# Kernel optimization log

Hardware: AMD Instinct MI355X
Metric: run time of the kernel (lower is better)

## Reference

```python
import jax, jax.numpy as jnp
import numpy as np
from jax import lax

L, C, H, W = 3, 64, 32, 32   # layer_num, new_size channels/spatial
N = H * W                    # 1024 attention positions
B = 8


def _conv(x, w, b, stride, pad):
    out = lax.conv_general_dilated(
        x, w, (stride, stride), [(pad, pad), (pad, pad)],
        dimension_numbers=('NCHW', 'OIHW', 'NCHW'))
    return out + b[None, :, None, None]


def setup_inputs() -> dict:
    key = jax.random.key(0)
    ks = iter(jax.random.split(key, 40))
    def rn(shape, scale=1.0):
        return (jax.random.normal(next(ks), shape) * scale).astype(jnp.float32)
    inp = {
        'src0': rn((B, 128, 64, 64)), 'src1': rn((B, 256, 32, 32)), 'src2': rn((B, 512, 32, 32)),
        'tgt0': rn((B, 128, 64, 64)), 'tgt1': rn((B, 256, 32, 32)), 'tgt2': rn((B, 512, 32, 32)),
    }
    # Project/Fit convs: layer0 is stride-2 3x3 (64->32), layers 1,2 are 1x1
    for pre, ic, k in [('fs0', 128, 3), ('fs1', 256, 1), ('fs2', 512, 1),
                       ('ft0', 128, 3), ('ft1', 256, 1), ('ft2', 512, 1)]:
        inp[pre + '_w'] = rn((C, ic, k, k), (ic * k * k) ** -0.5)
        inp[pre + '_b'] = rn((C,), 0.01)
    # PAM query/key/value and CAM value 1x1 convs, stacked over layers
    for pre in ['pq', 'pk', 'pv', 'cv']:
        inp[pre + '_w'] = rn((L, C, C), C ** -0.5)
        inp[pre + '_b'] = rn((L, C), 0.01)
    return inp


def reference(src0, src1, src2, tgt0, tgt1, tgt2,
              fs0_w, fs0_b, fs1_w, fs1_b, fs2_w, fs2_b,
              ft0_w, ft0_b, ft1_w, ft1_b, ft2_w, ft2_b,
              pq_w, pq_b, pk_w, pk_b, pv_w, pv_b, cv_w, cv_b):
    # Project: Fit each source/target to [B,C,H,W]
    S = jnp.stack([_conv(src0, fs0_w, fs0_b, 2, 1),
                   _conv(src1, fs1_w, fs1_b, 1, 0),
                   _conv(src2, fs2_w, fs2_b, 1, 0)])   # [L,B,C,H,W]
    T = jnp.stack([_conv(tgt0, ft0_w, ft0_b, 2, 1),
                   _conv(tgt1, ft1_w, ft1_b, 1, 0),
                   _conv(tgt2, ft2_w, ft2_b, 1, 0)])
    S = S.reshape(L, B, C, N)
    T = T.reshape(L, B, C, N)

    # ---- PAM: position attention over all (target i, source j) pairs ----
    q = jnp.einsum('ioc,ibcn->ibon', pq_w, T) + pq_b[:, None, :, None]
    k = jnp.einsum('joc,jbcn->jbon', pk_w, S) + pk_b[:, None, :, None]
    v = jnp.einsum('ioc,ibcn->ibon', pv_w, T) + pv_b[:, None, :, None]
    e_pam = jnp.einsum('ibcn,jbcm->ijbnm', q, k)          # [L,L,B,N,N]
    alpha_pam = jax.nn.softmax(lax.stop_gradient(e_pam.mean(axis=(2, 3, 4))), axis=-1)
    attn_pam = jax.nn.softmax(e_pam, axis=-1).sum(axis=1)  # sum over sources j -> [L,B,N,N]
    # out[b,c,n] = sum_m v[b,c,m] * attn[b,n,m]  (value @ attention^T)
    out_pam = jnp.einsum('ibcm,ibnm->ibcn', v, attn_pam)

    # ---- CAM: channel attention over all pairs ----
    e_cam = jnp.einsum('ibcn,jbdn->ijbcd', T, S)           # [L,L,B,C,C]
    alpha_cam = jax.nn.softmax(lax.stop_gradient(e_cam.mean(axis=(2, 3, 4))), axis=-1)
    attn_cam = jax.nn.softmax(e_cam, axis=-1).sum(axis=1)  # [L,B,C,C]
    vc = jnp.einsum('ioc,ibcn->ibon', cv_w, T) + cv_b[:, None, :, None]
    out_cam = jnp.einsum('ibcd,ibdn->ibcn', attn_cam, vc)

    fused = ((out_pam + out_cam) * 0.5).reshape(L, B, C * N)
    alpha = (alpha_cam + alpha_pam) * 0.5                  # [L,L]
    srcs = S.reshape(L, B, C * N)
    # DAAttention appends fused_i then projected target_i per layer (order preserved)
    tgts = jnp.stack([fused, T.reshape(L, B, C * N)], axis=1).reshape(2 * L, B, C * N)
    return (srcs, alpha, tgts)
```

## Files before the change

kernel.cpp:

```cpp
#include <hip/hip_runtime.h>

static constexpr int L_ = 3, B_ = 8, C_ = 64, N_ = 1024;
static constexpr int PLANE = C_ * N_;
static constexpr int SZ    = L_ * B_ * PLANE;
static constexpr int BPL   = B_ * PLANE;

#define DI __device__ __forceinline__

typedef _Float16 h8 __attribute__((ext_vector_type(8)));
typedef __attribute__((ext_vector_type(4))) float f32x4;
typedef unsigned int uint32;

DI float wred_sum(float v) {
#pragma unroll
  for (int m = 1; m < 64; m <<= 1) v += __shfl_xor(v, m, 64);
  return v;
}

DI unsigned short f2h(float f) {
  return __builtin_bit_cast(unsigned short, (_Float16)f);
}
DI float h2f(unsigned short h) {
  return (float)__builtin_bit_cast(_Float16, h);
}
DI uint32 pkh(float a, float b) {
  return (uint32)f2h(a) | ((uint32)f2h(b) << 16);
}
DI h8 bch8(uint4 v) { return __builtin_bit_cast(h8, v); }

DI f32x4 mfmah(h8 a, h8 b, f32x4 c) {
  return __builtin_amdgcn_mfma_f32_16x16x32_f16(a, b, c, 0, 0, 0);
}

__global__ __launch_bounds__(256) void xprep_kernel(
    const float* __restrict__ in, unsigned short* __restrict__ out, int K, int N)
{
  const int g = blockIdx.x, kc = blockIdx.y, nc = blockIdx.z;
  const int t = threadIdx.x;
  __shared__ float tl[64][65];
  const float* ing = in + (size_t)g * K * N + (size_t)(kc * 64) * N + nc * 64;
#pragma unroll 4
  for (int r = 0; r < 16; ++r) {
    const int kk = r * 4 + (t >> 6);
    tl[kk][t & 63] = ing[(size_t)kk * N + (t & 63)];
  }
  __syncthreads();
  const int mm = t >> 2, kseg = (t & 3) * 16;
  uint32 hw[8];
#pragma unroll
  for (int ii = 0; ii < 8; ++ii)
    hw[ii] = pkh(tl[kseg + 2 * ii][mm], tl[kseg + 2 * ii + 1][mm]);
  unsigned short* o = out + ((size_t)g * N + nc * 64 + mm) * K + kc * 64 + kseg;
  uint4 h0; h0.x = hw[0]; h0.y = hw[1]; h0.z = hw[2]; h0.w = hw[3];
  uint4 h1; h1.x = hw[4]; h1.y = hw[5]; h1.z = hw[6]; h1.w = hw[7];
  *reinterpret_cast<uint4*>(o)     = h0;
  *reinterpret_cast<uint4*>(o + 8) = h1;
}

__global__ __launch_bounds__(256) void w9conv_kernel(
    const float* __restrict__ w_s, const float* __restrict__ w_t,
    unsigned short* __restrict__ w9_s, unsigned short* __restrict__ w9_t)
{
  const int e = blockIdx.x * 256 + threadIdx.x;
  const float* w = (e < 73728) ? w_s : w_t;
  unsigned short* o = (e < 73728) ? w9_s : w9_t;
  const int le = (e < 73728) ? e : e - 73728;
  const int ci = le & 127;
  const int q = le >> 7;
  const int co = q & 63;
  const int k9 = q >> 6;
  o[le] = f2h(w[(co * 128 + ci) * 9 + k9]);
}

__global__ __launch_bounds__(256) void conv0_mfma_kernel(
    const unsigned short* __restrict__ inT_s, const unsigned short* __restrict__ inT_t,
    const unsigned short* __restrict__ w9_s, const unsigned short* __restrict__ w9_t,
    const float* __restrict__ b_s, const float* __restrict__ b_t,
    float* __restrict__ Sout, float* __restrict__ Tout, float* __restrict__ tdup)
{
  const int yr = blockIdx.x;
  const int b  = blockIdx.y;
  const int st = blockIdx.z;
  const unsigned short* inT = st ? inT_t : inT_s;
  const unsigned short* w9  = st ? w9_t  : w9_s;
  const float* bias = st ? b_t : b_s;
  float* outA = st ? Tout : Sout;

  const int t = threadIdx.x, lane = t & 63;
  const int ct = t >> 6;
  const int nl = lane & 15, g16 = lane >> 4;
  const unsigned short* inb = inT + (size_t)b * (4096 * 128);
  const unsigned short* wbase = w9 + (size_t)(ct * 16 + nl) * 128;

  f32x4 acc0 = f32x4{0.f, 0.f, 0.f, 0.f};
  f32x4 acc1 = f32x4{0.f, 0.f, 0.f, 0.f};
  const uint4 zz = uint4{0u, 0u, 0u, 0u};

#pragma unroll 1
  for (int tap = 0; tap < 9; ++tap) {
    const int ky = tap / 3, kx = tap - 3 * (tap / 3);
    const int py = 2 * yr - 1 + ky;
    const int px0 = 2 * nl - 1 + kx;
    const int px1 = px0 + 32;
    const bool v0 = (py >= 0) && (px0 >= 0);
    const bool v1 = (py >= 0);
    const unsigned short* prow = inb + (ptrdiff_t)py * (64 * 128);
#pragma unroll
    for (int ks = 0; ks < 4; ++ks) {
      const h8 a = bch8(*reinterpret_cast<const uint4*>(
          wbase + tap * 8192 + ks * 32 + g16 * 8));
      const uint4 bv0 = v0 ? *reinterpret_cast<const uint4*>(
                                 prow + px0 * 128 + ks * 32 + g16 * 8) : zz;
      const uint4 bv1 = v1 ? *reinterpret_cast<const uint4*>(
                                 prow + px1 * 128 + ks * 32 + g16 * 8) : zz;
      acc0 = mfmah(a, bch8(bv0), acc0);
      acc1 = mfmah(a, bch8(bv1), acc1);
    }
  }

  const int yb = yr * 32;
#pragma unroll
  for (int r = 0; r < 4; ++r) {
    const int co = ct * 16 + g16 * 4 + r;
    const float bv = bias[co];
    const int idx = (b * 64 + co) * 1024 + yb + nl;
    const float o0 = acc0[r] + bv;
    const float o1 = acc1[r] + bv;
    outA[idx] = o0; outA[idx + 16] = o1;
    if (st) { tdup[idx] = o0; tdup[idx + 16] = o1; }
  }
}

__global__ __launch_bounds__(256) void gemm64_kernel(
    const float* __restrict__ W, int wstride, int wdiv,
    const float* __restrict__ X, int xstride,
    float* __restrict__ out, int ostride,
    const float* __restrict__ bias, int bstride,
    int K)
{
  const int g  = blockIdx.x;
  const int n0 = blockIdx.y * 64;
  const float* Wg = W + (size_t)(g / wdiv) * wstride;
  const float* Xg = X + (size_t)g * xstride;
  const int t = threadIdx.x;
  __shared__ float Xs[32][64];
  __shared__ float Ws[32][64];
  const int tn = t & 15, cgp = t >> 4;
  const int n4 = tn * 4, co4 = cgp * 4;
  float acc[4][4] = {};

  for (int k0 = 0; k0 < K; k0 += 32) {
    {
      const int kk = t >> 4;
      const int nn = (t & 15) * 4;
      *reinterpret_cast<float4*>(&Xs[kk][nn]) =
          *reinterpret_cast<const float4*>(Xg + (size_t)(k0 + kk) * N_ + n0 + nn);
      *reinterpret_cast<float4*>(&Xs[kk + 16][nn]) =
          *reinterpret_cast<const float4*>(Xg + (size_t)(k0 + kk + 16) * N_ + n0 + nn);
    }
    {
      const int co = t & 63, q4 = t >> 6;
      const float* wp = Wg + (size_t)co * K + k0 + q4 * 8;
      const float4 a = *reinterpret_cast<const float4*>(wp);
      const float4 c = *reinterpret_cast<const float4*>(wp + 4);
      const int kb = q4 * 8;
      Ws[kb + 0][co] = a.x; Ws[kb + 1][co] = a.y; Ws[kb + 2][co] = a.z; Ws[kb + 3][co] = a.w;
      Ws[kb + 4][co] = c.x; Ws[kb + 5][co] = c.y; Ws[kb + 6][co] = c.z; Ws[kb + 7][co] = c.w;
    }
    __syncthreads();
#pragma unroll
    for (int kk = 0; kk < 32; ++kk) {
      const float4 xv = *reinterpret_cast<const float4*>(&Xs[kk][n4]);
      const float4 wv = *reinterpret_cast<const float4*>(&Ws[kk][co4]);
      const float xa[4] = {xv.x, xv.y, xv.z, xv.w};
      const float wa[4] = {wv.x, wv.y, wv.z, wv.w};
#pragma unroll
      for (int a = 0; a < 4; ++a)
#pragma unroll
        for (int b2 = 0; b2 < 4; ++b2)
          acc[a][b2] = fmaf(wa[a], xa[b2], acc[a][b2]);
    }
    __syncthreads();
  }

  float bv[4] = {0.f, 0.f, 0.f, 0.f};
  if (bias) {
    const float* bg = bias + (size_t)(g / wdiv) * bstride;
    bv[0] = bg[co4]; bv[1] = bg[co4 + 1]; bv[2] = bg[co4 + 2]; bv[3] = bg[co4 + 3];
  }
#pragma unroll
  for (int ii = 0; ii < 4; ++ii) {
    float4 o4;
    o4.x = acc[ii][0] + bv[ii]; o4.y = acc[ii][1] + bv[ii];
    o4.z = acc[ii][2] + bv[ii]; o4.w = acc[ii][3] + bv[ii];
    *reinterpret_cast<float4*>(out + (size_t)g * ostride + (co4 + ii) * N_ + n0 + n4) = o4;
  }
}

__global__ __launch_bounds__(256) void proj_kernel(
    const float* __restrict__ Tm, const float* __restrict__ Sm,
    const float* __restrict__ wq, const float* __restrict__ wk,
    const float* __restrict__ wv2, const float* __restrict__ wc,
    const float* __restrict__ bq, const float* __restrict__ bk,
    const float* __restrict__ bv2, const float* __restrict__ bc,
    float* __restrict__ outbase)
{
  const int g  = blockIdx.x;
  const int n0 = blockIdx.y * 64;
  const int z  = blockIdx.z;
  const float* W  = (z == 0) ? wq : (z == 1) ? wk : (z == 2) ? wv2 : wc;
  const float* bi = (z == 0) ? bq : (z == 1) ? bk : (z == 2) ? bv2 : bc;
  const float* Xg = ((z == 1) ? Sm : Tm) + (size_t)g * PLANE;
  float* out = outbase + (size_t)z * SZ + (size_t)g * PLANE;
  const float* Wg = W + (g >> 3) * 4096;
  const float* bg = bi + (g >> 3) * 64;

  const int t = threadIdx.x;
  __shared__ float Xs[32][64];
  __shared__ float Ws[32][64];
  const int tn = t & 15, cgp = t >> 4;
  const int n4 = tn * 4, co4 = cgp * 4;
  float acc[4][4] = {};

#pragma unroll 1
  for (int k0 = 0; k0 < 64; k0 += 32) {
    {
      const int kk = t >> 4;
      const int nn = (t & 15) * 4;
      *reinterpret_cast<float4*>(&Xs[kk][nn]) =
          *reinterpret_cast<const float4*>(Xg + (size_t)(k0 + kk) * N_ + n0 + nn);
      *reinterpret_cast<float4*>(&Xs[kk + 16][nn]) =
          *reinterpret_cast<const float4*>(Xg + (size_t)(k0 + kk + 16) * N_ + n0 + nn);
    }
    {
      const int co = t & 63, q4 = t >> 6;
      const float* wp = Wg + (size_t)co * 64 + k0 + q4 * 8;
      const float4 a = *reinterpret_cast<const float4*>(wp);
      const float4 c = *reinterpret_cast<const float4*>(wp + 4);
      const int kb = q4 * 8;
      Ws[kb + 0][co] = a.x; Ws[kb + 1][co] = a.y; Ws[kb + 2][co] = a.z; Ws[kb + 3][co] = a.w;
      Ws[kb + 4][co] = c.x; Ws[kb + 5][co] = c.y; Ws[kb + 6][co] = c.z; Ws[kb + 7][co] = c.w;
    }
    __syncthreads();
#pragma unroll
    for (int kk = 0; kk < 32; ++kk) {
      const float4 xv = *reinterpret_cast<const float4*>(&Xs[kk][n4]);
      const float4 wv = *reinterpret_cast<const float4*>(&Ws[kk][co4]);
      const float xa[4] = {xv.x, xv.y, xv.z, xv.w};
      const float wa[4] = {wv.x, wv.y, wv.z, wv.w};
#pragma unroll
      for (int a = 0; a < 4; ++a)
#pragma unroll
        for (int b2 = 0; b2 < 4; ++b2)
          acc[a][b2] = fmaf(wa[a], xa[b2], acc[a][b2]);
    }
    __syncthreads();
  }

#pragma unroll
  for (int ii = 0; ii < 4; ++ii) {
    const float bv = bg[co4 + ii];
    float4 o4;
    o4.x = acc[ii][0] + bv; o4.y = acc[ii][1] + bv;
    o4.z = acc[ii][2] + bv; o4.w = acc[ii][3] + bv;
    *reinterpret_cast<float4*>(out + (co4 + ii) * N_ + n0 + n4) = o4;
  }
}

__global__ __launch_bounds__(256) void whconv_kernel(
    const float* __restrict__ w1s, const float* __restrict__ w2s,
    const float* __restrict__ w1t, const float* __restrict__ w2t,
    unsigned short* __restrict__ wh)
{
  const int p = blockIdx.x * 256 + threadIdx.x;
  const float* in; int local; unsigned short* out;
  if (p < 8192)       { in = w1s; local = p;         out = wh; }
  else if (p < 24576) { in = w2s; local = p - 8192;  out = wh + 16384; }
  else if (p < 32768) { in = w1t; local = p - 24576; out = wh + 49152; }
  else                { in = w2t; local = p - 32768; out = wh + 65536; }
  const float2 v = *reinterpret_cast<const float2*>(in + 2 * local);
  *reinterpret_cast<uint32*>(out + 2 * local) = pkh(v.x, v.y);
}

__global__ __launch_bounds__(256) void gemmh_kernel(
    const unsigned short* __restrict__ Xa, const unsigned short* __restrict__ Xb,
    const unsigned short* __restrict__ Wa, const unsigned short* __restrict__ Wb,
    const float* __restrict__ ba, const float* __restrict__ bb,
    float* __restrict__ oa, float* __restrict__ ob, float* __restrict__ o2b,
    int K)
{
  const int g = blockIdx.x;
  const bool isb = g >= 8;
  const int gl = g & 7;
  const unsigned short* X = (isb ? Xb : Xa) + (size_t)gl * 1024 * K;
  const unsigned short* W = isb ? Wb : Wa;
  const float* bias = isb ? bb : ba;
  float* out = (isb ? ob : oa) + (size_t)gl * PLANE;
  float* out2 = isb ? o2b + (size_t)gl * PLANE : nullptr;

  const int t = threadIdx.x, lane = t & 63, wv = t >> 6;
  const int nl = lane & 15, g16 = lane >> 4;
  const int n0w = blockIdx.y * 64 + wv * 16;

  const unsigned short* xp = X + (size_t)(n0w + nl) * K + g16 * 8;
  const unsigned short* wp = W + (size_t)nl * K + g16 * 8;

  f32x4 acc[4];
#pragma unroll
  for (int ct = 0; ct < 4; ++ct) acc[ct] = f32x4{0.f, 0.f, 0.f, 0.f};

#pragma unroll 4
  for (int kk = 0; kk < K; kk += 32) {
    const h8 a = bch8(*reinterpret_cast<const uint4*>(xp + kk));
#pragma unroll
    for (int ct = 0; ct < 4; ++ct) {
      const h8 bfr = bch8(*reinterpret_cast<const uint4*>(wp + (size_t)ct * 16 * K + kk));
      acc[ct] = mfmah(a, bfr, acc[ct]);
    }
  }

#pragma unroll
  for (int ct = 0; ct < 4; ++ct) {
    const int co = ct * 16 + nl;
    const float bv = bias[co];
    float4 o4;
    o4.x = acc[ct][0] + bv; o4.y = acc[ct][1] + bv;
    o4.z = acc[ct][2] + bv; o4.w = acc[ct][3] + bv;
    const int idx = co * N_ + n0w + g16 * 4;
    *reinterpret_cast<float4*>(out + idx) = o4;
    if (out2) {
      out2[idx] = o4.x; out2[idx + 1] = o4.y;
      out2[idx + 2] = o4.z; out2[idx + 3] = o4.w;
    }
  }
}

__global__ __launch_bounds__(256) void kprep_kernel(
    const float* __restrict__ kb, const float* __restrict__ vb,
    unsigned short* __restrict__ kT, unsigned short* __restrict__ vh)
{
  const int g = blockIdx.x;
  const int ch = blockIdx.y;
  const int t = threadIdx.x;
  const float* kg = kb + (size_t)g * PLANE;
  __shared__ float tl[64][65];

#pragma unroll 1
  for (int tile = 0; tile < 4; ++tile) {
    const int m0 = ch * 256 + tile * 64;
    __syncthreads();
#pragma unroll 4
    for (int r = 0; r < 16; ++r) {
      const int c = r * 4 + (t >> 6);
      tl[c][t & 63] = kg[c * N_ + m0 + (t & 63)];
    }
    __syncthreads();
    const int mm = t >> 2, cseg = (t & 3) * 16;
    uint32 hw[8];
#pragma unroll
    for (int ii = 0; ii < 8; ++ii)
      hw[ii] = pkh(tl[cseg + 2 * ii][mm], tl[cseg + 2 * ii + 1][mm]);
    const size_t o = ((size_t)g * 1024 + m0 + mm) * 64 + cseg;
    uint4 h0; h0.x = hw[0]; h0.y = hw[1]; h0.z = hw[2]; h0.w = hw[3];
    uint4 h1; h1.x = hw[4]; h1.y = hw[5]; h1.z = hw[6]; h1.w = hw[7];
    *reinterpret_cast<uint4*>(kT + o)     = h0;
    *reinterpret_cast<uint4*>(kT + o + 8) = h1;
  }

  const float* vg = vb + (size_t)g * PLANE;
  unsigned short* vo = vh + (size_t)g * PLANE;
  for (int e8 = ch * 2048 + t; e8 < (ch + 1) * 2048; e8 += 256) {
    const float4 a = *reinterpret_cast<const float4*>(vg + (size_t)e8 * 8);
    const float4 b = *reinterpret_cast<const float4*>(vg + (size_t)e8 * 8 + 4);
    uint4 u;
    u.x = pkh(a.x, a.y); u.y = pkh(a.z, a.w);
    u.z = pkh(b.x, b.y); u.w = pkh(b.z, b.w);
    *reinterpret_cast<uint4*>(vo + (size_t)e8 * 8) = u;
  }
}

__global__ __launch_bounds__(256) void ecam_kernel(
    const float* __restrict__ T, const float* __restrict__ S,
    float* __restrict__ ecam, float* __restrict__ esum_cam)
{
  const int bx = blockIdx.x;
  const int b = bx & 7;
  const int j = (bx >> 3) % 3;
  const int i = bx / 24;
  const float* Tg = T + (size_t)(i * 8 + b) * PLANE;
  const float* Sg = S + (size_t)(j * 8 + b) * PLANE;
  const int t = threadIdx.x;
  __shared__ float Ts[64 * 68];
  __shared__ float Ss[64 * 68];
  __shared__ float rs[4];
  float acc[4][4] = {};
  const int c0 = (t & 15) * 4, d0 = (t >> 4) * 4;

  for (int nb = 0; nb < 1024; nb += 64) {
    __syncthreads();
    {
      const int nn = t & 63, rb = t >> 6;
#pragma unroll
      for (int r = 0; r < 16; ++r) {
        const int row = rb * 16 + r;
        Ts[nn * 68 + row] = Tg[row * N_ + nb + nn];
        Ss[nn * 68 + row] = Sg[row * N_ + nb + nn];
      }
    }
    __syncthreads();
#pragma unroll 8
    for (int nn = 0; nn < 64; ++nn) {
      const float4 tv = *reinterpret_cast<const float4*>(&Ts[nn * 68 + c0]);
      const float4 sv = *reinterpret_cast<const float4*>(&Ss[nn * 68 + d0]);
      const float ta[4] = {tv.x, tv.y, tv.z, tv.w};
      const float sa[4] = {sv.x, sv.y, sv.z, sv.w};
#pragma unroll
      for (int ci = 0; ci < 4; ++ci)
#pragma unroll
        for (int di = 0; di < 4; ++di)
          acc[ci][di] = fmaf(ta[ci], sa[di], acc[ci][di]);
    }
  }
  float s = 0.f;
#pragma unroll
  for (int ci = 0; ci < 4; ++ci)
#pragma unroll
    for (int di = 0; di < 4; ++di) s += acc[ci][di];
  s = wred_sum(s);
  if ((t & 63) == 0) rs[t >> 6] = s;
  __syncthreads();
  if (t == 0) atomicAdd(esum_cam + i * 3 + j, rs[0] + rs[1] + rs[2] + rs[3]);

  float* eo = ecam + (size_t)((i * 3 + j) * 8 + b) * 4096;
#pragma unroll
  for (int ci = 0; ci < 4; ++ci) {
    float4 o4; o4.x = acc[ci][0]; o4.y = acc[ci][1]; o4.z = acc[ci][2]; o4.w = acc[ci][3];
    *reinterpret_cast<float4*>(eo + (c0 + ci) * 64 + d0) = o4;
  }
}

__global__ __launch_bounds__(256) void acam_kernel(
    const float* __restrict__ ecam, float* __restrict__ acam)
{
  const int bx = blockIdx.x;
  const int b = bx & 7, i = bx >> 3;
  const int t = threadIdx.x;
  const int c = t >> 2, seg = t & 3;
  float acc[16] = {};
#pragma unroll
  for (int j = 0; j < 3; ++j) {
    const float* e = ecam + (size_t)((i * 3 + j) * 8 + b) * 4096 + c * 64 + seg * 16;
    float ev[16];
#pragma unroll
    for (int r = 0; r < 4; ++r) {
      const float4 v4 = *reinterpret_cast<const float4*>(e + r * 4);
      ev[4 * r] = v4.x; ev[4 * r + 1] = v4.y; ev[4 * r + 2] = v4.z; ev[4 * r + 3] = v4.w;
    }
    float mx = ev[0];
#pragma unroll
    for (int r = 1; r < 16; ++r) mx = fmaxf(mx, ev[r]);
    mx = fmaxf(mx, __shfl_xor(mx, 1, 4));
    mx = fmaxf(mx, __shfl_xor(mx, 2, 4));
    float pv[16], ss = 0.f;
#pragma unroll
    for (int r = 0; r < 16; ++r) { pv[r] = __expf(ev[r] - mx); ss += pv[r]; }
    ss += __shfl_xor(ss, 1, 4);
    ss += __shfl_xor(ss, 2, 4);
    const float rc = 1.f / ss;
#pragma unroll
    for (int r = 0; r < 16; ++r) acc[r] += pv[r] * rc;
  }
  float* ao = acam + (size_t)(i * 8 + b) * 4096 + c * 64 + seg * 16;
#pragma unroll
  for (int r = 0; r < 4; ++r) {
    float4 o4; o4.x = acc[4 * r]; o4.y = acc[4 * r + 1]; o4.z = acc[4 * r + 2]; o4.w = acc[4 * r + 3];
    *reinterpret_cast<float4*>(ao + r * 4) = o4;
  }
}

__global__ __launch_bounds__(512, 4) void pam_mfma_kernel(
    const float* __restrict__ q, const unsigned short* __restrict__ kT,
    const unsigned short* __restrict__ vh,
    const float* __restrict__ ocam, float* __restrict__ tgts, float* __restrict__ esum_pam)
{
  const int bx = blockIdx.x;
  const int qt = bx & 63;
  const int b  = (bx >> 6) & 7;
  const int i  = bx >> 9;
  const int n0 = qt * 16;
  const int t = threadIdx.x;
  const int lane = t & 63;
  const int wv = t >> 6;
  const int nl = lane & 15;
  const int g16 = lane >> 4;

  __shared__ unsigned short Plds[16 * 1024];
  __shared__ float qlds[64 * 17];
  __shared__ float redmx[128];
  __shared__ float redse[128];
  __shared__ float redes[8];
  float* osum = qlds;

  const size_t ibo = (size_t)(i * 8 + b) * PLANE;

  const float* qg = q + ibo;
  for (int e = t; e < 1024; e += 512)
    qlds[(e >> 4) * 17 + (e & 15)] = qg[(e >> 4) * N_ + n0 + (e & 15)];
  __syncthreads();

  h8 qh[2];
#pragma unroll
  for (int ks = 0; ks < 2; ++ks) {
#pragma unroll
    for (int idx = 0; idx < 8; ++idx)
      qh[ks][idx] = (_Float16)qlds[(ks * 32 + g16 * 8 + idx) * 17 + nl];
  }

  const int wm0 = wv * 128;
  const int ct = wv & 3;
  const int mh = wv >> 2;

#pragma unroll 1
  for (int j = 0; j < 3; ++j) {
    const unsigned short* kp =
        kT + ((size_t)(j * 8 + b) * 1024 + wm0 + nl) * 64 + g16 * 8;

    f32x4 l4[8];
#pragma unroll
    for (int hh = 0; hh < 2; ++hh) {
      uint4 kf[8];
#pragma unroll
      for (int tt = 0; tt < 4; ++tt) {
        const int off = (hh * 4 + tt) * 1024;
        kf[2 * tt]     = *reinterpret_cast<const uint4*>(kp + off);
        kf[2 * tt + 1] = *reinterpret_cast<const uint4*>(kp + off + 32);
      }
#pragma unroll
      for (int tt = 0; tt < 4; ++tt) {
        f32x4 a = f32x4{0.f, 0.f, 0.f, 0.f};
        a = mfmah(bch8(kf[2 * tt]), qh[0], a);
        a = mfmah(bch8(kf[2 * tt + 1]), qh[1], a);
        l4[hh * 4 + tt] = a;
      }
    }

    float pm = -3.4e38f, es = 0.f;
#pragma unroll
    for (int tt = 0; tt < 8; ++tt) {
#pragma unroll
      for (int r = 0; r < 4; ++r) { pm = fmaxf(pm, l4[tt][r]); es += l4[tt][r]; }
    }
    pm = fmaxf(pm, __shfl_xor(pm, 16, 64));
    pm = fmaxf(pm, __shfl_xor(pm, 32, 64));
    es = wred_sum(es);
    if (lane < 16) redmx[wv * 16 + lane] = pm;
    if (lane == 0) redes[wv] = es;
    __syncthreads();
    float mx = redmx[nl];
#pragma unroll
    for (int w = 1; w < 8; ++w) mx = fmaxf(mx, redmx[w * 16 + nl]);
    if (t == 0) {
      float s = 0.f;
#pragma unroll
      for (int w = 0; w < 8; ++w) s += redes[w];
      atomicAdd(esum_pam + i * 3 + j, s);
    }

    float ps = 0.f;
#pragma unroll
    for (int tt = 0; tt < 8; ++tt) {
#pragma unroll
      for (int r = 0; r < 4; ++r) {
        l4[tt][r] = __expf(l4[tt][r] - mx);
        ps += l4[tt][r];
      }
    }
    ps += __shfl_xor(ps, 16, 64);
    ps += __shfl_xor(ps, 32, 64);
    if (lane < 16) redse[wv * 16 + lane] = ps;
    __syncthreads();
    float den = redse[nl];
#pragma unroll
    for (int w = 1; w < 8; ++w) den += redse[w * 16 + nl];
    const float rs = 1.f / den;

#pragma unroll
    for (int tt = 0; tt < 8; ++tt) {
      const int m = wm0 + tt * 16 + g16 * 4;
      unsigned short* pp = &Plds[nl * 1024 + (m ^ (nl * 8))];
      float p0 = l4[tt][0] * rs, p1 = l4[tt][1] * rs;
      float p2 = l4[tt][2] * rs, p3 = l4[tt][3] * rs;
      if (j > 0) {
        const uint2 old = *reinterpret_cast<const uint2*>(pp);
        p0 += h2f((unsigned short)(old.x & 0xffffu));
        p1 += h2f((unsigned short)(old.x >> 16));
        p2 += h2f((unsigned short)(old.y & 0xffffu));
        p3 += h2f((unsigned short)(old.y >> 16));
      }
      uint2 w2; w2.x = pkh(p0, p1); w2.y = pkh(p2, p3);
      *reinterpret_cast<uint2*>(pp) = w2;
    }
  }

  __syncthreads();

  const unsigned short* vg = vh + ibo + (size_t)(ct * 16 + nl) * 1024 + mh * 512 + g16 * 8;
  f32x4 oa = f32x4{0.f, 0.f, 0.f, 0.f};
#pragma unroll
  for (int hh = 0; hh < 2; ++hh) {
    uint4 vf[8];
#pragma unroll
    for (int u = 0; u < 8; ++u)
      vf[u] = *reinterpret_cast<const uint4*>(vg + (hh * 8 + u) * 32);
#pragma unroll
    for (int u = 0; u < 8; ++u) {
      const int ml = mh * 512 + (hh * 8 + u) * 32 + g16 * 8;
      const uint4 pf = *reinterpret_cast<const uint4*>(&Plds[nl * 1024 + (ml ^ (nl * 8))]);
      oa = mfmah(bch8(vf[u]), bch8(pf), oa);
    }
  }

  if (mh == 0) {
#pragma unroll
    for (int r = 0; r < 4; ++r)
      osum[(ct * 16 + g16 * 4 + r) * 16 + nl] = oa[r];
  }
  __syncthreads();
  if (mh == 1) {
    const float* og = ocam + ibo;
    float* outg = tgts + (size_t)(2 * i * 8 + b) * PLANE;
#pragma unroll
    for (int r = 0; r < 4; ++r) {
      const int c = ct * 16 + g16 * 4 + r;
      const int idx = c * N_ + n0 + nl;
      outg[idx] = 0.5f * (oa[r] + osum[c * 16 + nl] + og[idx]);
    }
  }
}

__global__ void alpha_kernel(const float* __restrict__ esum, float* __restrict__ alpha)
{
  const int t = threadIdx.x;
  if (t >= 9) return;
  const int i = t / 3, j = t % 3;
  float p[3], c[3];
#pragma unroll
  for (int jj = 0; jj < 3; ++jj) {
    p[jj] = esum[i * 3 + jj] * (1.0f / 8388608.0f);
    c[jj] = esum[9 + i * 3 + jj] * (1.0f / 32768.0f);
  }
  const float mp = fmaxf(p[0], fmaxf(p[1], p[2]));
  const float mc = fmaxf(c[0], fmaxf(c[1], c[2]));
  float sp = 0.f, sc = 0.f;
#pragma unroll
  for (int jj = 0; jj < 3; ++jj) { sp += __expf(p[jj] - mp); sc += __expf(c[jj] - mc); }
  alpha[t] = 0.5f * (__expf(p[j] - mp) / sp + __expf(c[j] - mc) / sc);
}

extern "C" void kernel_launch(void* const* d_in, const int* in_sizes, int n_in,
                              void* d_out, int out_size, void* d_ws, size_t ws_size,
                              hipStream_t stream)
{
  const float* src0 = (const float*)d_in[0];
  const float* src1 = (const float*)d_in[1];
  const float* src2 = (const float*)d_in[2];
  const float* tgt0 = (const float*)d_in[3];
  const float* tgt1 = (const float*)d_in[4];
  const float* tgt2 = (const float*)d_in[5];
  const float* fs0_w = (const float*)d_in[6];  const float* fs0_b = (const float*)d_in[7];
  const float* fs1_w = (const float*)d_in[8];  const float* fs1_b = (const float*)d_in[9];
  const float* fs2_w = (const float*)d_in[10]; const float* fs2_b = (const float*)d_in[11];
  const float* ft0_w = (const float*)d_in[12]; const float* ft0_b = (const float*)d_in[13];
  const float* ft1_w = (const float*)d_in[14]; const float* ft1_b = (const float*)d_in[15];
  const float* ft2_w = (const float*)d_in[16]; const float* ft2_b = (const float*)d_in[17];
  const float* pq_w = (const float*)d_in[18];  const float* pq_b = (const float*)d_in[19];
  const float* pk_w = (const float*)d_in[20];  const float* pk_b = (const float*)d_in[21];
  const float* pv_w = (const float*)d_in[22];  const float* pv_b = (const float*)d_in[23];
  const float* cv_w = (const float*)d_in[24];  const float* cv_b = (const float*)d_in[25];

  float* out = (float*)d_out;
  float* S     = out;
  float* alpha = out + SZ;
  float* tgts  = out + SZ + 9;

  float* ws   = (float*)d_ws;
  float* T    = ws;
  float* qb   = ws + (size_t)SZ;
  float* kb   = ws + (size_t)2 * SZ;
  float* vb   = ws + (size_t)3 * SZ;
  float* vcb  = ws + (size_t)4 * SZ;
  float* ocam = ws + (size_t)5 * SZ;
  float* ecam = ws + (size_t)6 * SZ;
  float* acam = ws + (size_t)6 * SZ + 294912;
  float* esum = ws + (size_t)6 * SZ + 393216;

  unsigned short* kT = (unsigned short*)(ws + (size_t)6 * SZ + 393216 + 256);
  unsigned short* vh = kT + (size_t)24 * PLANE;
  unsigned short* wh = vh + (size_t)24 * PLANE;
  unsigned short* w9s = wh + 98304;
  unsigned short* w9t = w9s + 73728;

  unsigned short* inTs = (unsigned short*)qb;
  unsigned short* inTt = inTs + 4194304;
  unsigned short* Xs1 = (unsigned short*)qb;
  unsigned short* Xs2 = Xs1 + 2097152;
  unsigned short* Xt1 = Xs1 + 6291456;
  unsigned short* Xt2 = Xs1 + 8388608;

  hipMemsetAsync(esum, 0, 18 * sizeof(float), stream);

  w9conv_kernel<<<576, 256, 0, stream>>>(fs0_w, ft0_w, w9s, w9t);
  xprep_kernel<<<dim3(8, 2, 64), 256, 0, stream>>>(src0, inTs, 128, 4096);
  xprep_kernel<<<dim3(8, 2, 64), 256, 0, stream>>>(tgt0, inTt, 128, 4096);
  conv0_mfma_kernel<<<dim3(32, 8, 2), 256, 0, stream>>>(
      inTs, inTt, w9s, w9t, fs0_b, ft0_b, S, T, tgts + (size_t)1 * BPL);

  xprep_kernel<<<dim3(8, 4, 16), 256, 0, stream>>>(src1, Xs1, 256, 1024);
  xprep_kernel<<<dim3(8, 8, 16), 256, 0, stream>>>(src2, Xs2, 512, 1024);
  xprep_kernel<<<dim3(8, 4, 16), 256, 0, stream>>>(tgt1, Xt1, 256, 1024);
  xprep_kernel<<<dim3(8, 8, 16), 256, 0, stream>>>(tgt2, Xt2, 512, 1024);
  whconv_kernel<<<192, 256, 0, stream>>>(fs1_w, fs2_w, ft1_w, ft2_w, wh);
  gemmh_kernel<<<dim3(16, 16), 256, 0, stream>>>(
      Xs1, Xt1, wh, wh + 49152, fs1_b, ft1_b,
      S + BPL, T + BPL, tgts + (size_t)3 * BPL, 256);
  gemmh_kernel<<<dim3(16, 16), 256, 0, stream>>>(
      Xs2, Xt2, wh + 16384, wh + 65536, fs2_b, ft2_b,
      S + 2 * BPL, T + 2 * BPL, tgts + (size_t)5 * BPL, 512);

  proj_kernel<<<dim3(24, 16, 4), 256, 0, stream>>>(
      T, S, pq_w, pk_w, pv_w, cv_w, pq_b, pk_b, pv_b, cv_b, qb);

  kprep_kernel<<<dim3(24, 4), 256, 0, stream>>>(kb, vb, kT, vh);

  ecam_kernel<<<72, 256, 0, stream>>>(T, S, ecam, esum + 9);
  acam_kernel<<<24, 256, 0, stream>>>(ecam, acam);
  gemm64_kernel<<<dim3(24, 16), 256, 0, stream>>>(acam, 4096, 1, vcb, PLANE, ocam, PLANE,
                                                  nullptr, 0, 64);

  pam_mfma_kernel<<<1536, 512, 0, stream>>>(qb, kT, vh, ocam, tgts, esum);

  alpha_kernel<<<1, 64, 0, stream>>>(esum, alpha);
}
```

Measured before the change: 327.8 us.

## Fuse fp16 transpose into projection, merge xprep launches, split ecam with atomics

The projection kernel now writes q and k directly as transposed fp16 and v as fp16, so the separate kprep pass and the fp32 q/k/v round-trip through memory go away. The attention kernel now loads q fragments straight from the fp16 transposed buffer instead of staging fp32 through LDS. The six xprep launches collapse into two, and ecam is split four ways along N with atomicAdd accumulation, which needs an extra memset of the ecam buffer. This cuts launch count and memory traffic, at the cost of atomic contention and float atomics making the summation order non-deterministic.

```diff
diff --git a/kernel.cpp b/kernel.cpp
--- a/kernel.cpp
+++ b/kernel.cpp
@@ -32,13 +32,9 @@
   return __builtin_amdgcn_mfma_f32_16x16x32_f16(a, b, c, 0, 0, 0);
 }
 
-__global__ __launch_bounds__(256) void xprep_kernel(
-    const float* __restrict__ in, unsigned short* __restrict__ out, int K, int N)
-{
-  const int g = blockIdx.x, kc = blockIdx.y, nc = blockIdx.z;
-  const int t = threadIdx.x;
-  __shared__ float tl[64][65];
-  const float* ing = in + (size_t)g * K * N + (size_t)(kc * 64) * N + nc * 64;
+DI void xprep_body(const float* __restrict__ ing, unsigned short* __restrict__ og,
+                   int K, int N, int t, float tl[64][65])
+{
 #pragma unroll 4
   for (int r = 0; r < 16; ++r) {
     const int kk = r * 4 + (t >> 6);
@@ -50,11 +46,43 @@
 #pragma unroll
   for (int ii = 0; ii < 8; ++ii)
     hw[ii] = pkh(tl[kseg + 2 * ii][mm], tl[kseg + 2 * ii + 1][mm]);
-  unsigned short* o = out + ((size_t)g * N + nc * 64 + mm) * K + kc * 64 + kseg;
+  unsigned short* o = og + (size_t)mm * K + kseg;
   uint4 h0; h0.x = hw[0]; h0.y = hw[1]; h0.z = hw[2]; h0.w = hw[3];
   uint4 h1; h1.x = hw[4]; h1.y = hw[5]; h1.z = hw[6]; h1.w = hw[7];
   *reinterpret_cast<uint4*>(o)     = h0;
   *reinterpret_cast<uint4*>(o + 8) = h1;
+}
+
+__global__ __launch_bounds__(256) void xprep_conv_kernel(
+    const float* __restrict__ in_s, const float* __restrict__ in_t,
+    unsigned short* __restrict__ o_s, unsigned short* __restrict__ o_t)
+{
+  __shared__ float tl[64][65];
+  const int g = blockIdx.x & 7, ts = blockIdx.x >> 3;
+  const int kc = blockIdx.y, nc = blockIdx.z;
+  const float* in = ts ? in_t : in_s;
+  unsigned short* out = ts ? o_t : o_s;
+  const float* ing = in + (size_t)g * 128 * 4096 + (size_t)(kc * 64) * 4096 + nc * 64;
+  unsigned short* og = out + ((size_t)g * 4096 + nc * 64) * 128 + kc * 64;
+  xprep_body(ing, og, 128, 4096, threadIdx.x, tl);
+}
+
+__global__ __launch_bounds__(256) void xprep_fit_kernel(
+    const float* __restrict__ s1, const float* __restrict__ s2,
+    const float* __restrict__ t1, const float* __restrict__ t2,
+    unsigned short* __restrict__ x1, unsigned short* __restrict__ x2,
+    unsigned short* __restrict__ x3, unsigned short* __restrict__ x4)
+{
+  __shared__ float tl[64][65];
+  const int g = blockIdx.x & 7, ts = blockIdx.x >> 3;
+  const int K = (ts & 1) ? 512 : 256;
+  const int kc = blockIdx.y, nc = blockIdx.z;
+  if (kc >= (K >> 6)) return;
+  const float* in = (ts == 0) ? s1 : (ts == 1) ? s2 : (ts == 2) ? t1 : t2;
+  unsigned short* out = (ts == 0) ? x1 : (ts == 1) ? x2 : (ts == 2) ? x3 : x4;
+  const float* ing = in + (size_t)g * K * 1024 + (size_t)(kc * 64) * 1024 + nc * 64;
+  unsigned short* og = out + ((size_t)g * 1024 + nc * 64) * K + kc * 64;
+  xprep_body(ing, og, K, 1024, threadIdx.x, tl);
 }
 
 __global__ __launch_bounds__(256) void w9conv_kernel(
@@ -203,7 +231,8 @@
     const float* __restrict__ wv2, const float* __restrict__ wc,
     const float* __restrict__ bq, const float* __restrict__ bk,
     const float* __restrict__ bv2, const float* __restrict__ bc,
-    float* __restrict__ outbase)
+    unsigned short* __restrict__ qT, unsigned short* __restrict__ kT,
+    unsigned short* __restrict__ vh, float* __restrict__ vcb)
 {
   const int g  = blockIdx.x;
   const int n0 = blockIdx.y * 64;
@@ -211,7 +240,6 @@
   const float* W  = (z == 0) ? wq : (z == 1) ? wk : (z == 2) ? wv2 : wc;
   const float* bi = (z == 0) ? bq : (z == 1) ? bk : (z == 2) ? bv2 : bc;
   const float* Xg = ((z == 1) ? Sm : Tm) + (size_t)g * PLANE;
-  float* out = outbase + (size_t)z * SZ + (size_t)g * PLANE;
   const float* Wg = W + (g >> 3) * 4096;
   const float* bg = bi + (g >> 3) * 64;
 
@@ -257,13 +285,38 @@
     __syncthreads();
   }
 
-#pragma unroll
-  for (int ii = 0; ii < 4; ++ii) {
-    const float bv = bg[co4 + ii];
-    float4 o4;
-    o4.x = acc[ii][0] + bv; o4.y = acc[ii][1] + bv;
-    o4.z = acc[ii][2] + bv; o4.w = acc[ii][3] + bv;
-    *reinterpret_cast<float4*>(out + (co4 + ii) * N_ + n0 + n4) = o4;
+  float bvv[4];
+#pragma unroll
+  for (int ii = 0; ii < 4; ++ii) bvv[ii] = bg[co4 + ii];
+
+  if (z <= 1) {
+    unsigned short* out = (z == 0 ? qT : kT);
+#pragma unroll
+    for (int jj = 0; jj < 4; ++jj) {
+      const size_t base = ((size_t)g * 1024 + n0 + n4 + jj) * 64 + co4;
+      uint2 w2;
+      w2.x = pkh(acc[0][jj] + bvv[0], acc[1][jj] + bvv[1]);
+      w2.y = pkh(acc[2][jj] + bvv[2], acc[3][jj] + bvv[3]);
+      *reinterpret_cast<uint2*>(out + base) = w2;
+    }
+  } else if (z == 2) {
+#pragma unroll
+    for (int ii = 0; ii < 4; ++ii) {
+      const size_t base = ((size_t)g * 64 + co4 + ii) * 1024 + n0 + n4;
+      uint2 w2;
+      w2.x = pkh(acc[ii][0] + bvv[ii], acc[ii][1] + bvv[ii]);
+      w2.y = pkh(acc[ii][2] + bvv[ii], acc[ii][3] + bvv[ii]);
+      *reinterpret_cast<uint2*>(vh + base) = w2;
+    }
+  } else {
+    float* out = vcb + (size_t)g * PLANE;
+#pragma unroll
+    for (int ii = 0; ii < 4; ++ii) {
+      float4 o4;
+      o4.x = acc[ii][0] + bvv[ii]; o4.y = acc[ii][1] + bvv[ii];
+      o4.z = acc[ii][2] + bvv[ii]; o4.w = acc[ii][3] + bvv[ii];
+      *reinterpret_cast<float4*>(out + (co4 + ii) * N_ + n0 + n4) = o4;
+    }
   }
 }
 
@@ -335,50 +388,6 @@
   }
 }
 
-__global__ __launch_bounds__(256) void kprep_kernel(
-    const float* __restrict__ kb, const float* __restrict__ vb,
-    unsigned short* __restrict__ kT, unsigned short* __restrict__ vh)
-{
-  const int g = blockIdx.x;
-  const int ch = blockIdx.y;
-  const int t = threadIdx.x;
-  const float* kg = kb + (size_t)g * PLANE;
-  __shared__ float tl[64][65];
-
-#pragma unroll 1
-  for (int tile = 0; tile < 4; ++tile) {
-    const int m0 = ch * 256 + tile * 64;
-    __syncthreads();
-#pragma unroll 4
-    for (int r = 0; r < 16; ++r) {
-      const int c = r * 4 + (t >> 6);
-      tl[c][t & 63] = kg[c * N_ + m0 + (t & 63)];
-    }
-    __syncthreads();
-    const int mm = t >> 2, cseg = (t & 3) * 16;
-    uint32 hw[8];
-#pragma unroll
-    for (int ii = 0; ii < 8; ++ii)
-      hw[ii] = pkh(tl[cseg + 2 * ii][mm], tl[cseg + 2 * ii + 1][mm]);
-    const size_t o = ((size_t)g * 1024 + m0 + mm) * 64 + cseg;
-    uint4 h0; h0.x = hw[0]; h0.y = hw[1]; h0.z = hw[2]; h0.w = hw[3];
-    uint4 h1; h1.x = hw[4]; h1.y = hw[5]; h1.z = hw[6]; h1.w = hw[7];
-    *reinterpret_cast<uint4*>(kT + o)     = h0;
-    *reinterpret_cast<uint4*>(kT + o + 8) = h1;
-  }
-
-  const float* vg = vb + (size_t)g * PLANE;
-  unsigned short* vo = vh + (size_t)g * PLANE;
-  for (int e8 = ch * 2048 + t; e8 < (ch + 1) * 2048; e8 += 256) {
-    const float4 a = *reinterpret_cast<const float4*>(vg + (size_t)e8 * 8);
-    const float4 b = *reinterpret_cast<const float4*>(vg + (size_t)e8 * 8 + 4);
-    uint4 u;
-    u.x = pkh(a.x, a.y); u.y = pkh(a.z, a.w);
-    u.z = pkh(b.x, b.y); u.w = pkh(b.z, b.w);
-    *reinterpret_cast<uint4*>(vo + (size_t)e8 * 8) = u;
-  }
-}
-
 __global__ __launch_bounds__(256) void ecam_kernel(
     const float* __restrict__ T, const float* __restrict__ S,
     float* __restrict__ ecam, float* __restrict__ esum_cam)
@@ -387,6 +396,7 @@
   const int b = bx & 7;
   const int j = (bx >> 3) % 3;
   const int i = bx / 24;
+  const int ych = blockIdx.y;
   const float* Tg = T + (size_t)(i * 8 + b) * PLANE;
   const float* Sg = S + (size_t)(j * 8 + b) * PLANE;
   const int t = threadIdx.x;
@@ -396,7 +406,7 @@
   float acc[4][4] = {};
   const int c0 = (t & 15) * 4, d0 = (t >> 4) * 4;
 
-  for (int nb = 0; nb < 1024; nb += 64) {
+  for (int nb = ych * 256; nb < ych * 256 + 256; nb += 64) {
     __syncthreads();
     {
       const int nn = t & 63, rb = t >> 6;
@@ -433,10 +443,10 @@
 
   float* eo = ecam + (size_t)((i * 3 + j) * 8 + b) * 4096;
 #pragma unroll
-  for (int ci = 0; ci < 4; ++ci) {
-    float4 o4; o4.x = acc[ci][0]; o4.y = acc[ci][1]; o4.z = acc[ci][2]; o4.w = acc[ci][3];
-    *reinterpret_cast<float4*>(eo + (c0 + ci) * 64 + d0) = o4;
-  }
+  for (int ci = 0; ci < 4; ++ci)
+#pragma unroll
+    for (int di = 0; di < 4; ++di)
+      atomicAdd(eo + (c0 + ci) * 64 + d0 + di, acc[ci][di]);
 }
 
 __global__ __launch_bounds__(256) void acam_kernel(
@@ -479,7 +489,7 @@
 }
 
 __global__ __launch_bounds__(512, 4) void pam_mfma_kernel(
-    const float* __restrict__ q, const unsigned short* __restrict__ kT,
+    const unsigned short* __restrict__ qT, const unsigned short* __restrict__ kT,
     const unsigned short* __restrict__ vh,
     const float* __restrict__ ocam, float* __restrict__ tgts, float* __restrict__ esum_pam)
 {
@@ -495,26 +505,17 @@
   const int g16 = lane >> 4;
 
   __shared__ unsigned short Plds[16 * 1024];
-  __shared__ float qlds[64 * 17];
+  __shared__ float osum[64 * 16];
   __shared__ float redmx[128];
   __shared__ float redse[128];
   __shared__ float redes[8];
-  float* osum = qlds;
 
   const size_t ibo = (size_t)(i * 8 + b) * PLANE;
-
-  const float* qg = q + ibo;
-  for (int e = t; e < 1024; e += 512)
-    qlds[(e >> 4) * 17 + (e & 15)] = qg[(e >> 4) * N_ + n0 + (e & 15)];
-  __syncthreads();
-
-  h8 qh[2];
-#pragma unroll
-  for (int ks = 0; ks < 2; ++ks) {
-#pragma unroll
-    for (int idx = 0; idx < 8; ++idx)
-      qh[ks][idx] = (_Float16)qlds[(ks * 32 + g16 * 8 + idx) * 17 + nl];
-  }
+  const size_t gbase = (size_t)(i * 8 + b) * 1024;
+
+  const unsigned short* qp = qT + (gbase + n0 + nl) * 64 + g16 * 8;
+  const h8 qh0 = bch8(*reinterpret_cast<const uint4*>(qp));
+  const h8 qh1 = bch8(*reinterpret_cast<const uint4*>(qp + 32));
 
   const int wm0 = wv * 128;
   const int ct = wv & 3;
@@ -538,8 +539,8 @@
 #pragma unroll
       for (int tt = 0; tt < 4; ++tt) {
         f32x4 a = f32x4{0.f, 0.f, 0.f, 0.f};
-        a = mfmah(bch8(kf[2 * tt]), qh[0], a);
-        a = mfmah(bch8(kf[2 * tt + 1]), qh[1], a);
+        a = mfmah(bch8(kf[2 * tt]), qh0, a);
+        a = mfmah(bch8(kf[2 * tt + 1]), qh1, a);
         l4[hh * 4 + tt] = a;
       }
     }
@@ -687,7 +688,6 @@
   float* T    = ws;
   float* qb   = ws + (size_t)SZ;
   float* kb   = ws + (size_t)2 * SZ;
-  float* vb   = ws + (size_t)3 * SZ;
   float* vcb  = ws + (size_t)4 * SZ;
   float* ocam = ws + (size_t)5 * SZ;
   float* ecam = ws + (size_t)6 * SZ;
@@ -699,6 +699,7 @@
   unsigned short* wh = vh + (size_t)24 * PLANE;
   unsigned short* w9s = wh + 98304;
   unsigned short* w9t = w9s + 73728;
+  unsigned short* qT = (unsigned short*)kb;
 
   unsigned short* inTs = (unsigned short*)qb;
   unsigned short* inTt = inTs + 4194304;
@@ -708,17 +709,15 @@
   unsigned short* Xt2 = Xs1 + 8388608;
 
   hipMemsetAsync(esum, 0, 18 * sizeof(float), stream);
+  hipMemsetAsync(ecam, 0, 294912 * sizeof(float), stream);
 
   w9conv_kernel<<<576, 256, 0, stream>>>(fs0_w, ft0_w, w9s, w9t);
-  xprep_kernel<<<dim3(8, 2, 64), 256, 0, stream>>>(src0, inTs, 128, 4096);
-  xprep_kernel<<<dim3(8, 2, 64), 256, 0, stream>>>(tgt0, inTt, 128, 4096);
+  xprep_conv_kernel<<<dim3(16, 2, 64), 256, 0, stream>>>(src0, tgt0, inTs, inTt);
   conv0_mfma_kernel<<<dim3(32, 8, 2), 256, 0, stream>>>(
       inTs, inTt, w9s, w9t, fs0_b, ft0_b, S, T, tgts + (size_t)1 * BPL);
 
-  xprep_kernel<<<dim3(8, 4, 16), 256, 0, stream>>>(src1, Xs1, 256, 1024);
-  xprep_kernel<<<dim3(8, 8, 16), 256, 0, stream>>>(src2, Xs2, 512, 1024);
-  xprep_kernel<<<dim3(8, 4, 16), 256, 0, stream>>>(tgt1, Xt1, 256, 1024);
-  xprep_kernel<<<dim3(8, 8, 16), 256, 0, stream>>>(tgt2, Xt2, 512, 1024);
+  xprep_fit_kernel<<<dim3(32, 8, 16), 256, 0, stream>>>(
+      src1, src2, tgt1, tgt2, Xs1, Xs2, Xt1, Xt2);
   whconv_kernel<<<192, 256, 0, stream>>>(fs1_w, fs2_w, ft1_w, ft2_w, wh);
   gemmh_kernel<<<dim3(16, 16), 256, 0, stream>>>(
       Xs1, Xt1, wh, wh + 49152, fs1_b, ft1_b,
@@ -728,16 +727,14 @@
       S + 2 * BPL, T + 2 * BPL, tgts + (size_t)5 * BPL, 512);
 
   proj_kernel<<<dim3(24, 16, 4), 256, 0, stream>>>(
-      T, S, pq_w, pk_w, pv_w, cv_w, pq_b, pk_b, pv_b, cv_b, qb);
-
-  kprep_kernel<<<dim3(24, 4), 256, 0, stream>>>(kb, vb, kT, vh);
-
-  ecam_kernel<<<72, 256, 0, stream>>>(T, S, ecam, esum + 9);
+      T, S, pq_w, pk_w, pv_w, cv_w, pq_b, pk_b, pv_b, cv_b, qT, kT, vh, vcb);
+
+  ecam_kernel<<<dim3(72, 4), 256, 0, stream>>>(T, S, ecam, esum + 9);
   acam_kernel<<<24, 256, 0, stream>>>(ecam, acam);
   gemm64_kernel<<<dim3(24, 16), 256, 0, stream>>>(acam, 4096, 1, vcb, PLANE, ocam, PLANE,
                                                   nullptr, 0, 64);
 
-  pam_mfma_kernel<<<1536, 512, 0, stream>>>(qb, kT, vh, ocam, tgts, esum);
+  pam_mfma_kernel<<<1536, 512, 0, stream>>>(qT, kT, vh, ocam, tgts, esum);
 
   alpha_kernel<<<1, 64, 0, stream>>>(esum, alpha);
 }
```

After: 296.8 us. 1.1x faster.
